# Kernel optimization log

Hardware: AMD Instinct MI355X
Metric: run time of the kernel (lower is better)

The kernel has to match this reference:

```python
import jax, jax.numpy as jnp
import numpy as np

BN_EPS = 1e-5


def _weight_mlp(off, Wh, bh, Wo, bo):
    # off: [Nout, k, 2] relative neighbor offsets -> [Nout, k, 9] interp coeffs
    h = jax.nn.relu(off @ Wh + bh)
    return h @ Wo + bo


def _interp_conv(x, idx, off, Wk, bk, Wh, bh, Wo, bo):
    # x: [B, Cin, Nin]; idx: [Nout, k] neighbor indices into Nin; Wk: [Cout, Cin, 9]
    a = _weight_mlp(off, Wh, bh, Wo, bo)        # [Nout, k, 9]
    feats = x[:, :, idx]                         # gather -> [B, Cin, Nout, k]
    # dynamic filter: per-neighbor kernel = a @ Wk taps, contracted with features
    y = jnp.einsum('nkt,bcnk,oct->bon', a, feats, Wk)  # [B, Cout, Nout]
    return y + bk[None, :, None]


def _bn_relu(x, g, b):
    # BatchNorm1d over [B, C, N] using batch statistics (training-mode forward)
    mean = x.mean(axis=(0, 2), keepdims=True)
    var = x.var(axis=(0, 2), keepdims=True)
    xn = (x - mean) * jax.lax.rsqrt(var + BN_EPS)
    return jax.nn.relu(xn * g[None, :, None] + b[None, :, None])


def setup_inputs() -> dict:
    key = jax.random.key(0)
    ks = jax.random.split(key, 12)
    B, N1, N2, N3, K = 8, 50176, 12544, 3136, 9
    inp = {
        'x': jax.random.normal(ks[0], (B, 3, N1), jnp.float32),
        'nbr1': jax.random.randint(ks[1], (N2, K), 0, N1, jnp.int32),
        'off1': jax.random.normal(ks[2], (N2, K, 2), jnp.float32),
        'nbr2': jax.random.randint(ks[3], (N2, K), 0, N2, jnp.int32),
        'off2': jax.random.normal(ks[4], (N2, K, 2), jnp.float32),
        'pool_idx': jax.random.randint(ks[5], (N3, K), 0, N2, jnp.int32),
        'Wh': jax.random.normal(ks[6], (2, 32), jnp.float32) * 0.5,
        'bh': jnp.zeros((32,), jnp.float32),
        'Wo': jax.random.normal(ks[7], (32, 9), jnp.float32) * 0.2,
        'bo': jnp.zeros((9,), jnp.float32),
        'W1': jax.random.normal(ks[8], (32, 3, 9), jnp.float32) * 0.2,
        'b1': jnp.zeros((32,), jnp.float32),
        'W2': jax.random.normal(ks[9], (32, 32, 9), jnp.float32) * 0.06,
        'b2': jnp.zeros((32,), jnp.float32),
        'W3': jax.random.normal(ks[10], (64, 32, 9), jnp.float32) * 0.06,
        'b3': jnp.zeros((64,), jnp.float32),
        'g1': jnp.ones((32,), jnp.float32), 'be1': jnp.zeros((32,), jnp.float32),
        'g2': jnp.ones((32,), jnp.float32), 'be2': jnp.zeros((32,), jnp.float32),
        'g3': jnp.ones((64,), jnp.float32), 'be3': jnp.zeros((64,), jnp.float32),
    }
    return inp


def reference(x, nbr1, off1, nbr2, off2, pool_idx, Wh, bh, Wo, bo,
              W1, b1, W2, b2, W3, b3, g1, be1, g2, be2, g3, be3):
    x = _bn_relu(_interp_conv(x, nbr1, off1, W1, b1, Wh, bh, Wo, bo), g1, be1)
    x = _bn_relu(_interp_conv(x, nbr2, off2, W2, b2, Wh, bh, Wo, bo), g2, be2)
    x = _bn_relu(_interp_conv(x, nbr2, off2, W3, b3, Wh, bh, Wo, bo), g3, be3)
    # MaxPoolNG: max over irregular neighbor sets from level l2 -> l3
    x = x[:, :, pool_idx].max(axis=-1)           # [B, 64, N3]
    return x
```

## Files before the change

### kernel.cpp

```cpp
#include <hip/hip_runtime.h>
#include <math.h>

#define N1C 50176
#define N2C 12544
#define N3C 3136
#define NT_TILES (N2C * 8 / 64)

typedef __attribute__((ext_vector_type(8))) short bf16x8;
typedef __attribute__((ext_vector_type(4))) float f32x4;

__device__ __forceinline__ unsigned short f2bf(float f) {
    unsigned u = __builtin_bit_cast(unsigned, f);
    u += 0x7fffu + ((u >> 16) & 1u);
    return (unsigned short)(u >> 16);
}
__device__ __forceinline__ unsigned packbf(float a, float b) {
    return (unsigned)f2bf(a) | ((unsigned)f2bf(b) << 16);
}
__device__ __forceinline__ float bf2f(unsigned short u) {
    return __builtin_bit_cast(float, (unsigned)u << 16);
}
__device__ __forceinline__ float bflo(unsigned u) {
    return __builtin_bit_cast(float, u << 16);
}
__device__ __forceinline__ float bfhi(unsigned u) {
    return __builtin_bit_cast(float, u & 0xffff0000u);
}

#define TRB (N1C / 64)
#define MLB (2 * N2C * 9 / 256)
#define PWB 112

__device__ __forceinline__ void pad_one(int i, const float* __restrict__ W,
                                        unsigned short* __restrict__ Wp,
                                        int OC, int CIN, int KT) {
    int j = i & 7;
    int op = (i >> 3) & 31;
    int q = (i >> 8) & 3;
    int kt = (i >> 10) % KT;
    int g = i / (KT * 1024);
    int kp = kt * 32 + q * 8 + j;
    int t = kp / CIN, c = kp - t * CIN;
    int o = g * 32 + op;
    float v = (t < 9 && o < OC) ? W[(o * CIN + c) * 9 + t] : 0.f;
    Wp[i] = f2bf(v);
}

__global__ void prologue_kernel(const float* __restrict__ x, unsigned short* __restrict__ X0,
                                const float* __restrict__ off1, const float* __restrict__ off2,
                                const float* __restrict__ Wh, const float* __restrict__ bh,
                                const float* __restrict__ Wo, const float* __restrict__ bo,
                                float* __restrict__ A1, float* __restrict__ A2,
                                const float* __restrict__ W1, const float* __restrict__ W2,
                                const float* __restrict__ W3,
                                unsigned short* __restrict__ W1p, unsigned short* __restrict__ W2p,
                                unsigned short* __restrict__ W3p) {
    __shared__ float U[2304];
    int blk = blockIdx.x;
    int tid = threadIdx.x;
    if (blk < TRB) {
        int n0 = blk * 64;
        for (int r = tid; r < 24 * 64; r += 256) {
            int cb = r >> 6;
            int nn = r & 63;
            U[nn * 25 + cb] = x[cb * N1C + n0 + nn];
        }
        __syncthreads();
        for (int w = tid; w < 64 * 24; w += 256) {
            int nn = w / 24;
            int u = w - nn * 24;
            X0[(n0 + nn) * 24 + u] = f2bf(U[nn * 25 + u]);
        }
    } else if (blk < TRB + MLB) {
        int bi = blk - TRB;
        int idx = bi * 256 + tid;
        const float* offp;
        if (idx < N2C * 9) offp = off1 + idx * 2;
        else offp = off2 + (idx - N2C * 9) * 2;
        float o0 = offp[0], o1 = offp[1];
        float out[9];
#pragma unroll
        for (int t = 0; t < 9; t++) out[t] = bo[t];
#pragma unroll
        for (int h = 0; h < 32; h++) {
            float hv = fmaxf(o0 * Wh[h] + o1 * Wh[32 + h] + bh[h], 0.f);
#pragma unroll
            for (int t = 0; t < 9; t++) out[t] += hv * Wo[h * 9 + t];
        }
#pragma unroll
        for (int t = 0; t < 9; t++) U[tid * 9 + t] = out[t];
        __syncthreads();
        float* dst = (bi < 441) ? (A1 + (size_t)bi * 2304)
                                : (A2 + (size_t)(bi - 441) * 2304);
        for (int i = tid; i < 2304; i += 256) dst[i] = U[i];
    } else {
        int i = (blk - TRB - MLB) * 256 + tid;
        if (i < 1024) pad_one(i, W1, W1p, 32, 3, 1);
        else if (i < 10240) pad_one(i - 1024, W2, W2p, 32, 32, 9);
        else pad_one(i - 10240, W3, W3p, 64, 32, 9);
    }
}

template <int CIN, int MW, bool HAS_BN>
__global__ __launch_bounds__(256, 4)
void conv_kernel(const unsigned short* __restrict__ Xin,
                 const int* __restrict__ nbr,
                 const float* __restrict__ A,
                 const unsigned short* __restrict__ Wp,
                 const float* __restrict__ bias,
                 const float* __restrict__ bnsc,
                 const float* __restrict__ bnsh,
                 unsigned short* __restrict__ Yb,
                 double* __restrict__ Part) {
    constexpr int OC = MW * 16;
    constexpr int KREAL = 9 * CIN;
    constexpr int KROW = (KREAL + 31) & ~31;
    constexpr int KT = KROW / 32;
    constexpr int KSTR = KROW + 8;
    constexpr int PARTS = 256 / OC;
    constexpr int PCOLS = 64 / PARTS;
    constexpr int OSH = (OC == 32) ? 5 : 6;
    constexpr int YSTR = OC + 4;
    constexpr int SB1 = 64 * KSTR * 2;
    constexpr int SB2 = 64 * YSTR * 4 + PARTS * 2 * OC * 4;
    constexpr int SBYTES = SB1 > SB2 ? SB1 : SB2;
    __shared__ alignas(16) char Sraw[SBYTES];
    __shared__ float a_lds[8 * 81];
    short* S = (short*)Sraw;

    int tid = threadIdx.x;
    int tile = blockIdx.x;
    int n0 = tile * 8;

    if constexpr (CIN == 3) {
        for (int i = tid; i < 64 * KSTR; i += 256) S[i] = 0;
        for (int i = tid; i < 648; i += 256) a_lds[i] = A[(size_t)n0 * 81 + i];
        __syncthreads();
        if (tid < 192) {
            int nsub = tid / 24;
            int u = tid - nsub * 24;
            int b = u / 3, c = u - b * 3;
            int n = n0 + nsub;
            const int* nb = nbr + n * 9;
            const float* Ar = a_lds + nsub * 81;
            float s[9];
#pragma unroll
            for (int t = 0; t < 9; t++) s[t] = 0.f;
#pragma unroll
            for (int k = 0; k < 9; k++) {
                float f = bf2f(Xin[nb[k] * 24 + u]);
#pragma unroll
                for (int t = 0; t < 9; t++) s[t] = fmaf(Ar[k * 9 + t], f, s[t]);
            }
            int col = nsub * 8 + b;
#pragma unroll
            for (int t = 0; t < 9; t++) S[col * KSTR + t * 3 + c] = (short)f2bf(s[t]);
        }
    } else {
        int wv4 = __builtin_amdgcn_readfirstlane(tid >> 6);
        int lane = tid & 63;
        int b = lane >> 3, c4 = lane & 7;
        float4 scv = {1.f, 1.f, 1.f, 1.f}, shv = {0.f, 0.f, 0.f, 0.f};
        if (HAS_BN) {
            scv = *(const float4*)&bnsc[4 * c4];
            shv = *(const float4*)&bnsh[4 * c4];
        }
        const uint2* Xd = (const uint2*)Xin;
        uint2 fu[18];
#pragma unroll
        for (int gg = 0; gg < 2; gg++)
#pragma unroll
            for (int k = 0; k < 9; k++) {
                int j = nbr[(n0 + wv4 * 2 + gg) * 9 + k];
                fu[gg * 9 + k] = Xd[(size_t)j * 64 + lane];
            }
        for (int i = tid; i < 648; i += 256) a_lds[i] = A[(size_t)n0 * 81 + i];
        __syncthreads();
#pragma unroll
        for (int gg = 0; gg < 2; gg++) {
            const float* Ar = a_lds + (wv4 * 2 + gg) * 81;
            float s0[9], s1[9], s2[9], s3[9];
#pragma unroll
            for (int t = 0; t < 9; t++) { s0[t] = 0.f; s1[t] = 0.f; s2[t] = 0.f; s3[t] = 0.f; }
#pragma unroll
            for (int k = 0; k < 9; k++) {
                uint2 u = fu[gg * 9 + k];
                float f0 = bflo(u.x), f1 = bfhi(u.x);
                float f2 = bflo(u.y), f3 = bfhi(u.y);
                if (HAS_BN) {
                    f0 = fmaxf(fmaf(f0, scv.x, shv.x), 0.f);
                    f1 = fmaxf(fmaf(f1, scv.y, shv.y), 0.f);
                    f2 = fmaxf(fmaf(f2, scv.z, shv.z), 0.f);
                    f3 = fmaxf(fmaf(f3, scv.w, shv.w), 0.f);
                }
#pragma unroll
                for (int t = 0; t < 9; t++) {
                    float a = Ar[k * 9 + t];
                    s0[t] = fmaf(a, f0, s0[t]);
                    s1[t] = fmaf(a, f1, s1[t]);
                    s2[t] = fmaf(a, f2, s2[t]);
                    s3[t] = fmaf(a, f3, s3[t]);
                }
            }
            int col = (wv4 * 2 + gg) * 8 + b;
            uint2* Srow = (uint2*)&S[col * KSTR];
#pragma unroll
            for (int t = 0; t < 9; t++) {
                uint2 pk;
                pk.x = packbf(s0[t], s1[t]);
                pk.y = packbf(s2[t], s3[t]);
                Srow[t * 8 + c4] = pk;
            }
        }
    }
    __syncthreads();

    int lane = tid & 63, wv = tid >> 6, q = lane >> 4, cl = lane & 15;
    int colg = wv * 16 + cl;

    const bf16x8* wf = (const bf16x8*)Wp;
    f32x4 acc[MW];
#pragma unroll
    for (int m = 0; m < MW; m++) acc[m] = (f32x4){0.f, 0.f, 0.f, 0.f};
#pragma unroll
    for (int kt = 0; kt < KT; kt++) {
        bf16x8 bfr = *(const bf16x8*)&S[colg * KSTR + kt * 32 + q * 8];
#pragma unroll
        for (int m = 0; m < MW; m++) {
            const bf16x8* wg = wf + (m >> 1) * (KT * 128);
            bf16x8 am = wg[(kt * 4 + q) * 32 + cl + (m & 1) * 16];
            acc[m] = __builtin_amdgcn_mfma_f32_16x16x32_bf16(am, bfr, acc[m], 0, 0, 0);
        }
    }
    __syncthreads();

    float* Yf = (float*)Sraw;
    float* P2f = Yf + 64 * YSTR;
    int C = tile * 64 + colg;
#pragma unroll
    for (int m = 0; m < MW; m++) {
        f32x4 v;
#pragma unroll
        for (int i = 0; i < 4; i++) v[i] = acc[m][i] + bias[m * 16 + q * 4 + i];
        *(f32x4*)&Yf[colg * YSTR + m * 16 + q * 4] = v;
        uint2 pk;
        pk.x = packbf(v[0], v[1]);
        pk.y = packbf(v[2], v[3]);
        *(uint2*)&Yb[(size_t)C * OC + m * 16 + q * 4] = pk;
    }
    __syncthreads();
    {
        int o = tid & (OC - 1);
        int part = tid >> OSH;
        float s = 0.f, qq = 0.f;
#pragma unroll
        for (int i = 0; i < PCOLS; i++) {
            float y = Yf[(part * PCOLS + i) * YSTR + o];
            s += y;
            qq += y * y;
        }
        P2f[part * 2 * OC + o] = s;
        P2f[part * 2 * OC + OC + o] = qq;
    }
    __syncthreads();
    if (tid < 2 * OC) {
        double v = 0.0;
#pragma unroll
        for (int p = 0; p < PARTS; p++) v += (double)P2f[p * 2 * OC + tid];
        Part[(size_t)tid * NT_TILES + tile] = v;
    }
}

__global__ __launch_bounds__(256, 8)
void bn_reduce(const double* __restrict__ Part,
               const float* __restrict__ g, const float* __restrict__ be,
               float* __restrict__ sc, float* __restrict__ sh, int OC) {
    int o = blockIdx.x;
    int tid = threadIdx.x;
    const double* ps = Part + (size_t)o * NT_TILES;
    const double* pq = Part + (size_t)(OC + o) * NT_TILES;
    double s = 0.0, q = 0.0;
    for (int t = tid; t < NT_TILES; t += 256) {
        s += ps[t];
        q += pq[t];
    }
#pragma unroll
    for (int d = 1; d < 64; d <<= 1) {
        s += __shfl_xor(s, d);
        q += __shfl_xor(q, d);
    }
    __shared__ double red[8];
    int wv = tid >> 6;
    if ((tid & 63) == 0) { red[wv] = s; red[4 + wv] = q; }
    __syncthreads();
    if (tid == 0) {
        double S = red[0] + red[1] + red[2] + red[3];
        double Q = red[4] + red[5] + red[6] + red[7];
        double cnt = (double)N2C * 8.0;
        double mean = S / cnt;
        double var = Q / cnt - mean * mean;
        double rs = 1.0 / sqrt(var + 1e-5);
        double scale = (double)g[o] * rs;
        sc[o] = (float)scale;
        sh[o] = (float)((double)be[o] - mean * scale);
    }
}

__global__ __launch_bounds__(256, 8)
void pool_kernel(const unsigned short* __restrict__ Y3, const int* __restrict__ pidx,
                 const float* __restrict__ sc, const float* __restrict__ sh,
                 float* __restrict__ out) {
    int m0 = blockIdx.x * 2;
    int tid = threadIdx.x;
    int o2 = tid & 31;
    int b = tid >> 5;
    float s0 = sc[2 * o2], h0 = sh[2 * o2];
    float s1 = sc[2 * o2 + 1], h1 = sh[2 * o2 + 1];
    const unsigned* Y3u = (const unsigned*)Y3;
    int j0[9], j1[9];
#pragma unroll
    for (int k = 0; k < 9; k++) {
        j0[k] = pidx[m0 * 9 + k];
        j1[k] = pidx[m0 * 9 + 9 + k];
    }
    unsigned u0[9], u1[9];
#pragma unroll
    for (int k = 0; k < 9; k++) u0[k] = Y3u[(size_t)j0[k] * 256 + tid];
#pragma unroll
    for (int k = 0; k < 9; k++) u1[k] = Y3u[(size_t)j1[k] * 256 + tid];
    float a0 = 0.f, a1 = 0.f, c0 = 0.f, c1 = 0.f;
#pragma unroll
    for (int k = 0; k < 9; k++) {
        a0 = fmaxf(a0, fmaf(bflo(u0[k]), s0, h0));
        a1 = fmaxf(a1, fmaf(bfhi(u0[k]), s1, h1));
        c0 = fmaxf(c0, fmaf(bflo(u1[k]), s0, h0));
        c1 = fmaxf(c1, fmaf(bfhi(u1[k]), s1, h1));
    }
    float2 r0 = {a0, c0};
    float2 r1 = {a1, c1};
    *(float2*)(out + (size_t)(b * 64 + 2 * o2) * 3136 + m0) = r0;
    *(float2*)(out + (size_t)(b * 64 + 2 * o2 + 1) * 3136 + m0) = r1;
}

extern "C" void kernel_launch(void* const* d_in, const int* in_sizes, int n_in,
                              void* d_out, int out_size, void* d_ws, size_t ws_size,
                              hipStream_t stream) {
    const float* x    = (const float*)d_in[0];
    const int*   nbr1 = (const int*)d_in[1];
    const float* off1 = (const float*)d_in[2];
    const int*   nbr2 = (const int*)d_in[3];
    const float* off2 = (const float*)d_in[4];
    const int*   pidx = (const int*)d_in[5];
    const float* Wh   = (const float*)d_in[6];
    const float* bh   = (const float*)d_in[7];
    const float* Wo   = (const float*)d_in[8];
    const float* bo   = (const float*)d_in[9];
    const float* W1   = (const float*)d_in[10];
    const float* b1   = (const float*)d_in[11];
    const float* W2   = (const float*)d_in[12];
    const float* b2   = (const float*)d_in[13];
    const float* W3   = (const float*)d_in[14];
    const float* b3   = (const float*)d_in[15];
    const float* g1   = (const float*)d_in[16];
    const float* be1  = (const float*)d_in[17];
    const float* g2   = (const float*)d_in[18];
    const float* be2  = (const float*)d_in[19];
    const float* g3   = (const float*)d_in[20];
    const float* be3  = (const float*)d_in[21];

    char* ws = (char*)d_ws;
    size_t off = 0;
    auto alloc = [&](size_t bytes) -> void* {
        void* p = ws + off;
        off += (bytes + 255) & ~(size_t)255;
        return p;
    };
    unsigned short* X0b = (unsigned short*)alloc((size_t)N1C * 24 * 2);
    float* A1 = (float*)alloc((size_t)N2C * 81 * 4);
    float* A2 = (float*)alloc((size_t)N2C * 81 * 4);
    unsigned short* Y1b = (unsigned short*)alloc((size_t)N2C * 8 * 32 * 2);
    unsigned short* Y2b = (unsigned short*)alloc((size_t)N2C * 8 * 32 * 2);
    unsigned short* Y3b = (unsigned short*)alloc((size_t)N2C * 8 * 64 * 2);
    unsigned short* W1p = (unsigned short*)alloc(32 * 32 * 2);
    unsigned short* W2p = (unsigned short*)alloc(32 * 288 * 2);
    unsigned short* W3p = (unsigned short*)alloc(64 * 288 * 2);
    double* Part  = (double*)alloc((size_t)NT_TILES * 128 * 8);
    float*  scbuf = (float*)alloc(256 * 4);

    float* sc1 = scbuf;       float* sh1 = scbuf + 32;
    float* sc2 = scbuf + 64;  float* sh2 = scbuf + 96;
    float* sc3 = scbuf + 128; float* sh3 = scbuf + 192;

    prologue_kernel<<<TRB + MLB + PWB, 256, 0, stream>>>(
        x, X0b, off1, off2, Wh, bh, Wo, bo, A1, A2, W1, W2, W3, W1p, W2p, W3p);

    conv_kernel<3, 2, false><<<NT_TILES, 256, 0, stream>>>(
        X0b, nbr1, A1, W1p, b1, nullptr, nullptr, Y1b, Part);
    bn_reduce<<<32, 256, 0, stream>>>(Part, g1, be1, sc1, sh1, 32);

    conv_kernel<32, 2, true><<<NT_TILES, 256, 0, stream>>>(
        Y1b, nbr2, A2, W2p, b2, sc1, sh1, Y2b, Part);
    bn_reduce<<<32, 256, 0, stream>>>(Part, g2, be2, sc2, sh2, 32);

    conv_kernel<32, 4, true><<<NT_TILES, 256, 0, stream>>>(
        Y2b, nbr2, A2, W3p, b3, sc2, sh2, Y3b, Part);
    bn_reduce<<<64, 256, 0, stream>>>(Part, g3, be3, sc3, sh3, 64);

    pool_kernel<<<N3C / 2, 256, 0, stream>>>(Y3b, pidx, sc3, sh3, (float*)d_out);
}
```

Measured before the change: 189.7 us.

## Software-pipeline 32-channel conv layers over two tiles per block

New measurement: 214.7 us. +13.2%, slower.

```diff
diff --git a/kernel.cpp b/kernel.cpp
--- a/kernel.cpp
+++ b/kernel.cpp
@@ -16,6 +16,11 @@
 }
 __device__ __forceinline__ unsigned packbf(float a, float b) {
     return (unsigned)f2bf(a) | ((unsigned)f2bf(b) << 16);
+}
+__device__ __forceinline__ unsigned cvtpk(float lo, float hi) {
+    unsigned r;
+    asm("v_cvt_pk_bf16_f32 %0, %1, %2" : "=v"(r) : "v"(lo), "v"(hi));
+    return r;
 }
 __device__ __forceinline__ float bf2f(unsigned short u) {
     return __builtin_bit_cast(float, (unsigned)u << 16);
@@ -132,86 +137,28 @@
     int tile = blockIdx.x;
     int n0 = tile * 8;
 
-    if constexpr (CIN == 3) {
-        for (int i = tid; i < 64 * KSTR; i += 256) S[i] = 0;
-        for (int i = tid; i < 648; i += 256) a_lds[i] = A[(size_t)n0 * 81 + i];
-        __syncthreads();
-        if (tid < 192) {
-            int nsub = tid / 24;
-            int u = tid - nsub * 24;
-            int b = u / 3, c = u - b * 3;
-            int n = n0 + nsub;
-            const int* nb = nbr + n * 9;
-            const float* Ar = a_lds + nsub * 81;
-            float s[9];
-#pragma unroll
-            for (int t = 0; t < 9; t++) s[t] = 0.f;
-#pragma unroll
-            for (int k = 0; k < 9; k++) {
-                float f = bf2f(Xin[nb[k] * 24 + u]);
-#pragma unroll
-                for (int t = 0; t < 9; t++) s[t] = fmaf(Ar[k * 9 + t], f, s[t]);
-            }
-            int col = nsub * 8 + b;
-#pragma unroll
-            for (int t = 0; t < 9; t++) S[col * KSTR + t * 3 + c] = (short)f2bf(s[t]);
-        }
-    } else {
-        int wv4 = __builtin_amdgcn_readfirstlane(tid >> 6);
-        int lane = tid & 63;
-        int b = lane >> 3, c4 = lane & 7;
-        float4 scv = {1.f, 1.f, 1.f, 1.f}, shv = {0.f, 0.f, 0.f, 0.f};
-        if (HAS_BN) {
-            scv = *(const float4*)&bnsc[4 * c4];
-            shv = *(const float4*)&bnsh[4 * c4];
-        }
-        const uint2* Xd = (const uint2*)Xin;
-        uint2 fu[18];
-#pragma unroll
-        for (int gg = 0; gg < 2; gg++)
-#pragma unroll
-            for (int k = 0; k < 9; k++) {
-                int j = nbr[(n0 + wv4 * 2 + gg) * 9 + k];
-                fu[gg * 9 + k] = Xd[(size_t)j * 64 + lane];
-            }
-        for (int i = tid; i < 648; i += 256) a_lds[i] = A[(size_t)n0 * 81 + i];
-        __syncthreads();
-#pragma unroll
-        for (int gg = 0; gg < 2; gg++) {
-            const float* Ar = a_lds + (wv4 * 2 + gg) * 81;
-            float s0[9], s1[9], s2[9], s3[9];
-#pragma unroll
-            for (int t = 0; t < 9; t++) { s0[t] = 0.f; s1[t] = 0.f; s2[t] = 0.f; s3[t] = 0.f; }
-#pragma unroll
-            for (int k = 0; k < 9; k++) {
-                uint2 u = fu[gg * 9 + k];
-                float f0 = bflo(u.x), f1 = bfhi(u.x);
-                float f2 = bflo(u.y), f3 = bfhi(u.y);
-                if (HAS_BN) {
-                    f0 = fmaxf(fmaf(f0, scv.x, shv.x), 0.f);
-                    f1 = fmaxf(fmaf(f1, scv.y, shv.y), 0.f);
-                    f2 = fmaxf(fmaf(f2, scv.z, shv.z), 0.f);
-                    f3 = fmaxf(fmaf(f3, scv.w, shv.w), 0.f);
-                }
-#pragma unroll
-                for (int t = 0; t < 9; t++) {
-                    float a = Ar[k * 9 + t];
-                    s0[t] = fmaf(a, f0, s0[t]);
-                    s1[t] = fmaf(a, f1, s1[t]);
-                    s2[t] = fmaf(a, f2, s2[t]);
-                    s3[t] = fmaf(a, f3, s3[t]);
-                }
-            }
-            int col = (wv4 * 2 + gg) * 8 + b;
-            uint2* Srow = (uint2*)&S[col * KSTR];
-#pragma unroll
-            for (int t = 0; t < 9; t++) {
-                uint2 pk;
-                pk.x = packbf(s0[t], s1[t]);
-                pk.y = packbf(s2[t], s3[t]);
-                Srow[t * 8 + c4] = pk;
-            }
-        }
+    for (int i = tid; i < 64 * KSTR; i += 256) S[i] = 0;
+    for (int i = tid; i < 648; i += 256) a_lds[i] = A[(size_t)n0 * 81 + i];
+    __syncthreads();
+    if (tid < 192) {
+        int nsub = tid / 24;
+        int u = tid - nsub * 24;
+        int b = u / 3, c = u - b * 3;
+        int n = n0 + nsub;
+        const int* nb = nbr + n * 9;
+        const float* Ar = a_lds + nsub * 81;
+        float s[9];
+#pragma unroll
+        for (int t = 0; t < 9; t++) s[t] = 0.f;
+#pragma unroll
+        for (int k = 0; k < 9; k++) {
+            float f = bf2f(Xin[nb[k] * 24 + u]);
+#pragma unroll
+            for (int t = 0; t < 9; t++) s[t] = fmaf(Ar[k * 9 + t], f, s[t]);
+        }
+        int col = nsub * 8 + b;
+#pragma unroll
+        for (int t = 0; t < 9; t++) S[col * KSTR + t * 3 + c] = (short)f2bf(s[t]);
     }
     __syncthreads();
 
@@ -244,8 +191,8 @@
         for (int i = 0; i < 4; i++) v[i] = acc[m][i] + bias[m * 16 + q * 4 + i];
         *(f32x4*)&Yf[colg * YSTR + m * 16 + q * 4] = v;
         uint2 pk;
-        pk.x = packbf(v[0], v[1]);
-        pk.y = packbf(v[2], v[3]);
+        pk.x = cvtpk(v[0], v[1]);
+        pk.y = cvtpk(v[2], v[3]);
         *(uint2*)&Yb[(size_t)C * OC + m * 16 + q * 4] = pk;
     }
     __syncthreads();
@@ -268,6 +215,158 @@
 #pragma unroll
         for (int p = 0; p < PARTS; p++) v += (double)P2f[p * 2 * OC + tid];
         Part[(size_t)tid * NT_TILES + tile] = v;
+    }
+}
+
+template <int MW>
+__global__ __launch_bounds__(256, 4)
+void conv32_kernel(const unsigned short* __restrict__ Xin,
+                   const int* __restrict__ nbr,
+                   const float* __restrict__ A,
+                   const unsigned short* __restrict__ Wp,
+                   const float* __restrict__ bias,
+                   const float* __restrict__ bnsc,
+                   const float* __restrict__ bnsh,
+                   unsigned short* __restrict__ Yb,
+                   double* __restrict__ Part) {
+    constexpr int OC = MW * 16;
+    constexpr int KROW = 288;
+    constexpr int KT = 9;
+    constexpr int KSTR = KROW + 8;
+    constexpr int PARTS = 256 / OC;
+    constexpr int PCOLS = 64 / PARTS;
+    constexpr int OSH = (OC == 32) ? 5 : 6;
+    constexpr int YSTR = OC + 4;
+    constexpr int SB1 = 64 * KSTR * 2;
+    constexpr int SB2 = 64 * YSTR * 4 + PARTS * 2 * OC * 4;
+    constexpr int SBYTES = SB1 > SB2 ? SB1 : SB2;
+    __shared__ alignas(16) char Sraw[SBYTES];
+    __shared__ float a_lds[8 * 81];
+    short* S = (short*)Sraw;
+
+    int tid = threadIdx.x;
+    int tile0 = blockIdx.x * 2;
+
+    int wv4 = __builtin_amdgcn_readfirstlane(tid >> 6);
+    int lane = tid & 63;
+    int b = lane >> 3, c4 = lane & 7;
+    float4 scv = *(const float4*)&bnsc[4 * c4];
+    float4 shv = *(const float4*)&bnsh[4 * c4];
+    const uint2* Xd = (const uint2*)Xin;
+
+    auto issue_half = [&](int tile, int gg, uint2* fu) {
+        int nb = (tile * 8 + wv4 * 2 + gg) * 9;
+#pragma unroll
+        for (int k = 0; k < 9; k++) {
+            int j = nbr[nb + k];
+            fu[k] = Xd[(size_t)j * 64 + lane];
+        }
+    };
+    auto stage_a = [&](int tile) {
+        for (int i = tid; i < 648; i += 256) a_lds[i] = A[(size_t)tile * 648 + i];
+    };
+    auto compute_half = [&](int gg, const uint2* fu) {
+        const float* Ar = a_lds + (wv4 * 2 + gg) * 81;
+        float s0[9], s1[9], s2[9], s3[9];
+#pragma unroll
+        for (int t = 0; t < 9; t++) { s0[t] = 0.f; s1[t] = 0.f; s2[t] = 0.f; s3[t] = 0.f; }
+#pragma unroll
+        for (int k = 0; k < 9; k++) {
+            uint2 u = fu[k];
+            float f0 = fmaxf(fmaf(bflo(u.x), scv.x, shv.x), 0.f);
+            float f1 = fmaxf(fmaf(bfhi(u.x), scv.y, shv.y), 0.f);
+            float f2 = fmaxf(fmaf(bflo(u.y), scv.z, shv.z), 0.f);
+            float f3 = fmaxf(fmaf(bfhi(u.y), scv.w, shv.w), 0.f);
+#pragma unroll
+            for (int t = 0; t < 9; t++) {
+                float a = Ar[k * 9 + t];
+                s0[t] = fmaf(a, f0, s0[t]);
+                s1[t] = fmaf(a, f1, s1[t]);
+                s2[t] = fmaf(a, f2, s2[t]);
+                s3[t] = fmaf(a, f3, s3[t]);
+            }
+        }
+        int col = (wv4 * 2 + gg) * 8 + b;
+        uint2* Srow = (uint2*)&S[col * KSTR];
+#pragma unroll
+        for (int t = 0; t < 9; t++) {
+            uint2 pk;
+            pk.x = cvtpk(s0[t], s1[t]);
+            pk.y = cvtpk(s2[t], s3[t]);
+            Srow[t * 8 + c4] = pk;
+        }
+    };
+
+    int wv = tid >> 6, q = lane >> 4, cl = lane & 15;
+    int colg = wv * 16 + cl;
+    const bf16x8* wf = (const bf16x8*)Wp;
+    float* Yf = (float*)Sraw;
+    float* P2f = Yf + 64 * YSTR;
+
+    uint2 fuA[9], fuB[9];
+    issue_half(tile0, 0, fuA);
+    stage_a(tile0);
+    __syncthreads();
+
+#pragma unroll 1
+    for (int it = 0; it < 2; ++it) {
+        int tile = tile0 + it;
+        issue_half(tile, 1, fuB);
+        compute_half(0, fuA);
+        compute_half(1, fuB);
+        __syncthreads();
+        if (it == 0) issue_half(tile0 + 1, 0, fuA);
+
+        f32x4 acc[MW];
+#pragma unroll
+        for (int m = 0; m < MW; m++) acc[m] = (f32x4){0.f, 0.f, 0.f, 0.f};
+#pragma unroll
+        for (int kt = 0; kt < KT; kt++) {
+            bf16x8 bfr = *(const bf16x8*)&S[colg * KSTR + kt * 32 + q * 8];
+#pragma unroll
+            for (int m = 0; m < MW; m++) {
+                const bf16x8* wg = wf + (m >> 1) * (KT * 128);
+                bf16x8 am = wg[(kt * 4 + q) * 32 + cl + (m & 1) * 16];
+                acc[m] = __builtin_amdgcn_mfma_f32_16x16x32_bf16(am, bfr, acc[m], 0, 0, 0);
+            }
+        }
+        __syncthreads();
+
+        int C = tile * 64 + colg;
+#pragma unroll
+        for (int m = 0; m < MW; m++) {
+            f32x4 v;
+#pragma unroll
+            for (int i = 0; i < 4; i++) v[i] = acc[m][i] + bias[m * 16 + q * 4 + i];
+            *(f32x4*)&Yf[colg * YSTR + m * 16 + q * 4] = v;
+            uint2 pk;
+            pk.x = cvtpk(v[0], v[1]);
+            pk.y = cvtpk(v[2], v[3]);
+            *(uint2*)&Yb[(size_t)C * OC + m * 16 + q * 4] = pk;
+        }
+        if (it == 0) stage_a(tile0 + 1);
+        __syncthreads();
+        {
+            int o = tid & (OC - 1);
+            int part = tid >> OSH;
+            float s = 0.f, qq = 0.f;
+#pragma unroll
+            for (int i = 0; i < PCOLS; i++) {
+                float y = Yf[(part * PCOLS + i) * YSTR + o];
+                s += y;
+                qq += y * y;
+            }
+            P2f[part * 2 * OC + o] = s;
+            P2f[part * 2 * OC + OC + o] = qq;
+        }
+        __syncthreads();
+        if (tid < 2 * OC) {
+            double v = 0.0;
+#pragma unroll
+            for (int p = 0; p < PARTS; p++) v += (double)P2f[p * 2 * OC + tid];
+            Part[(size_t)tid * NT_TILES + tile] = v;
+        }
+        if (it == 0) __syncthreads();
     }
 }
 
@@ -398,11 +497,11 @@
         X0b, nbr1, A1, W1p, b1, nullptr, nullptr, Y1b, Part);
     bn_reduce<<<32, 256, 0, stream>>>(Part, g1, be1, sc1, sh1, 32);
 
-    conv_kernel<32, 2, true><<<NT_TILES, 256, 0, stream>>>(
+    conv32_kernel<2><<<NT_TILES / 2, 256, 0, stream>>>(
         Y1b, nbr2, A2, W2p, b2, sc1, sh1, Y2b, Part);
     bn_reduce<<<32, 256, 0, stream>>>(Part, g2, be2, sc2, sh2, 32);
 
-    conv_kernel<32, 4, true><<<NT_TILES, 256, 0, stream>>>(
+    conv32_kernel<4><<<NT_TILES / 2, 256, 0, stream>>>(
         Y2b, nbr2, A2, W3p, b3, sc2, sh2, Y3b, Part);
     bn_reduce<<<64, 256, 0, stream>>>(Part, g3, be3, sc3, sh3, 64);
 
```
